# Performance work log

Hardware: AMD Instinct MI355X
Metric: run time of the kernel (lower is better)

Reference implementation:

```python
import jax, jax.numpy as jnp
import numpy as np

N_NODES = 100000
N_EDGES = 3200000


def setup_inputs() -> dict:
    key = jax.random.key(0)
    k1, k2, k3, k4, k5, k6, k7 = jax.random.split(key, 7)
    features = jax.random.normal(k1, (N_NODES, 1), dtype=jnp.float32)
    src = jax.random.randint(k2, (N_EDGES,), 0, N_NODES, dtype=jnp.int64)
    dst = jax.random.randint(k3, (N_EDGES,), 0, N_NODES, dtype=jnp.int64)
    # Linear layer params (PyTorch nn.Linear default init scale ~ 1/sqrt(fan_in))
    W1 = jax.random.normal(k4, (1, 16), dtype=jnp.float32)
    b1 = jax.random.normal(k5, (16,), dtype=jnp.float32) * 0.1
    W2 = jax.random.normal(k6, (16, 1), dtype=jnp.float32) * (1.0 / 4.0)
    b2 = jax.random.normal(k7, (1,), dtype=jnp.float32) * 0.1
    return {"features": features, "src": src, "dst": dst,
            "W1": W1, "b1": b1, "W2": W2, "b2": b2}


def _gcn_layer(h, src, dst, W, b):
    # DGL GCN: sum-aggregate neighbor features along edges, then Linear + ReLU.
    msgs = h[src]                                   # [E, d_in] gather
    agg = jax.ops.segment_sum(msgs, dst, num_segments=N_NODES)  # [N, d_in]
    return jax.nn.relu(agg @ W + b)                 # [N, d_out]


def reference(features, src, dst, W1, b1, W2, b2):
    h = _gcn_layer(features, src, dst, W1, b1)      # [N, 16]
    out = _gcn_layer(h, src, dst, W2, b2)           # [N, 1]
    return out
```

## Files before the change

kernel.cpp:

```cpp
#include <hip/hip_runtime.h>

#define NN 100000
#define NE 3200000
#define NQ (NE / 4)

#define NCHUNK 32
#define CHUNK 3125
#define NBB 512
#define BCAP 320
#define NSLICE 16
#define GPS (NBB / NSLICE)

__global__ __launch_bounds__(1024) void bucket_kernel(
        const int4* __restrict__ src4, const int4* __restrict__ dst4,
        unsigned* __restrict__ bkt, int* __restrict__ counts) {
    __shared__ int cnt[NCHUNK];
    if (threadIdx.x < NCHUNK) cnt[threadIdx.x] = 0;
    __syncthreads();
    const int b = blockIdx.x;
    const int q0 = (int)(((long long)b * NQ) / NBB);
    const int q1 = (int)(((long long)(b + 1) * NQ) / NBB);
    for (int q = q0 + threadIdx.x; q < q1; q += 1024) {
        const int4 d = dst4[q];
        const int4 s = src4[q];
        const int dd[4] = {d.x, d.y, d.z, d.w};
        const int ss[4] = {s.x, s.y, s.z, s.w};
#pragma unroll
        for (int j = 0; j < 4; ++j) {
            const int c = dd[j] / CHUNK;
            const int slot = atomicAdd(&cnt[c], 1);
            bkt[((size_t)c * NBB + b) * BCAP + slot] =
                ((unsigned)(dd[j] - c * CHUNK) << 17) | (unsigned)ss[j];
        }
    }
    __syncthreads();
    if (threadIdx.x < NCHUNK)
        counts[threadIdx.x * NBB + b] = cnt[threadIdx.x];
}

__global__ __launch_bounds__(1024) void scatter_bkt_kernel(
        const float* __restrict__ h,
        const unsigned* __restrict__ bkt, const int* __restrict__ counts,
        float* __restrict__ partial) {
    __shared__ float acc[CHUNK];
    const int s = blockIdx.x, c = blockIdx.y;
    for (int i = threadIdx.x; i < CHUNK; i += 1024) acc[i] = 0.0f;
    __syncthreads();
    const int lane = threadIdx.x & 63;
    const int w = threadIdx.x >> 6;
#pragma unroll
    for (int k = 0; k < 2; ++k) {
        const int b = s * GPS + w + k * 16;
        const int n = counts[c * NBB + b];
        const unsigned* bp = bkt + ((size_t)c * NBB + b) * BCAP;
        const uint4* bp4 = (const uint4*)bp;
        const int n4 = n >> 2;
        for (int q = lane; q < n4; q += 64) {
            const uint4 e = bp4[q];
            atomicAdd(&acc[e.x >> 17], h[e.x & 0x1FFFF]);
            atomicAdd(&acc[e.y >> 17], h[e.y & 0x1FFFF]);
            atomicAdd(&acc[e.z >> 17], h[e.z & 0x1FFFF]);
            atomicAdd(&acc[e.w >> 17], h[e.w & 0x1FFFF]);
        }
        const int base = n4 << 2;
        if (base + lane < n) {
            const unsigned e = bp[base + lane];
            atomicAdd(&acc[e >> 17], h[e & 0x1FFFF]);
        }
    }
    __syncthreads();
    float* out = partial + ((size_t)c * NSLICE + s) * CHUNK;
    for (int i = threadIdx.x; i < CHUNK; i += 1024) out[i] = acc[i];
}

__global__ __launch_bounds__(256) void reduce_mlp_kernel(
        const float* __restrict__ partial,
        const float* __restrict__ W1, const float* __restrict__ b1,
        const float* __restrict__ W2,
        float* __restrict__ sout, int n) {
    int i = blockIdx.x * blockDim.x + threadIdx.x;
    if (i >= n) return;
    const int c = i / CHUNK;
    const int idx = i - c * CHUNK;
    const float* base = partial + (size_t)c * NSLICE * CHUNK + idx;
    float a = 0.0f;
#pragma unroll
    for (int s = 0; s < NSLICE; ++s) a += base[(size_t)s * CHUNK];
    float r = 0.0f;
#pragma unroll
    for (int j = 0; j < 16; ++j)
        r = fmaf(fmaxf(fmaf(a, W1[j], b1[j]), 0.0f), W2[j], r);
    sout[i] = r;
}

__global__ __launch_bounds__(256) void reduce_final_kernel(
        const float* __restrict__ partial,
        const float* __restrict__ b2,
        float* __restrict__ out, int n) {
    int i = blockIdx.x * blockDim.x + threadIdx.x;
    if (i >= n) return;
    const int c = i / CHUNK;
    const int idx = i - c * CHUNK;
    const float* base = partial + (size_t)c * NSLICE * CHUNK + idx;
    float a = 0.0f;
#pragma unroll
    for (int s = 0; s < NSLICE; ++s) a += base[(size_t)s * CHUNK];
    out[i] = fmaxf(a + b2[0], 0.0f);
}

__global__ void zero_kernel(float* __restrict__ p, int n) {
    int i = blockIdx.x * blockDim.x + threadIdx.x;
    int st = gridDim.x * blockDim.x;
    for (; i < n; i += st) p[i] = 0.0f;
}
__global__ __launch_bounds__(256) void edge_scatter_kernel(
        const float* __restrict__ h, const int4* __restrict__ src4,
        const int4* __restrict__ dst4, float* __restrict__ agg, int nquad) {
    int i = blockIdx.x * blockDim.x + threadIdx.x;
    if (i >= nquad) return;
    int4 s = src4[i]; int4 d = dst4[i];
    atomicAdd(&agg[d.x], h[s.x]);
    atomicAdd(&agg[d.y], h[s.y]);
    atomicAdd(&agg[d.z], h[s.z]);
    atomicAdd(&agg[d.w], h[s.w]);
}
__global__ __launch_bounds__(256) void mlp_kernel(
        const float* __restrict__ agg1, const float* __restrict__ W1,
        const float* __restrict__ b1, const float* __restrict__ W2,
        float* __restrict__ sout, int n) {
    int i = blockIdx.x * blockDim.x + threadIdx.x;
    if (i >= n) return;
    float a = agg1[i], r = 0.0f;
#pragma unroll
    for (int j = 0; j < 16; ++j)
        r = fmaf(fmaxf(fmaf(a, W1[j], b1[j]), 0.0f), W2[j], r);
    sout[i] = r;
}
__global__ __launch_bounds__(256) void finalize_kernel(
        float* __restrict__ out, const float* __restrict__ b2, int n) {
    int i = blockIdx.x * blockDim.x + threadIdx.x;
    if (i >= n) return;
    out[i] = fmaxf(out[i] + b2[0], 0.0f);
}

extern "C" void kernel_launch(void* const* d_in, const int* in_sizes, int n_in,
                              void* d_out, int out_size, void* d_ws, size_t ws_size,
                              hipStream_t stream) {
    const float* features = (const float*)d_in[0];
    const int*   src      = (const int*)d_in[1];
    const int*   dst      = (const int*)d_in[2];
    const float* W1       = (const float*)d_in[3];
    const float* b1       = (const float*)d_in[4];
    const float* W2       = (const float*)d_in[5];
    const float* b2       = (const float*)d_in[6];
    float* out = (float*)d_out;

    const int nb = (NN + 255) / 256;

    {
        const size_t bkt_elems  = (size_t)NCHUNK * NBB * BCAP;
        const size_t cnt_elems  = (size_t)NCHUNK * NBB;
        const size_t part_elems = (size_t)NCHUNK * NSLICE * CHUNK;
        const size_t need = (bkt_elems + cnt_elems + part_elems + NN) * 4;
        if (ws_size >= need) {
            unsigned* bkt  = (unsigned*)d_ws;
            int* counts    = (int*)(bkt + bkt_elems);
            float* partial = (float*)(counts + cnt_elems);
            float* sbuf    = partial + part_elems;

            bucket_kernel<<<NBB, 1024, 0, stream>>>(
                (const int4*)src, (const int4*)dst, bkt, counts);
            dim3 g(NSLICE, NCHUNK);
            scatter_bkt_kernel<<<g, 1024, 0, stream>>>(features, bkt, counts, partial);
            reduce_mlp_kernel<<<nb, 256, 0, stream>>>(partial, W1, b1, W2, sbuf, NN);
            scatter_bkt_kernel<<<g, 1024, 0, stream>>>(sbuf, bkt, counts, partial);
            reduce_final_kernel<<<nb, 256, 0, stream>>>(partial, b2, out, NN);
            return;
        }
    }
    {
        float* agg1 = (float*)d_ws;
        float* sbuf = agg1 + NN;
        const int4* src4 = (const int4*)src;
        const int4* dst4 = (const int4*)dst;
        const int eb = (NQ + 255) / 256;
        zero_kernel<<<256, 256, 0, stream>>>(agg1, NN);
        edge_scatter_kernel<<<eb, 256, 0, stream>>>(features, src4, dst4, agg1, NQ);
        mlp_kernel<<<nb, 256, 0, stream>>>(agg1, W1, b1, W2, sbuf, NN);
        zero_kernel<<<256, 256, 0, stream>>>(out, NN);
        edge_scatter_kernel<<<eb, 256, 0, stream>>>(sbuf, src4, dst4, out, NQ);
        finalize_kernel<<<nb, 256, 0, stream>>>(out, b2, NN);
    }
}
```

Measured before the change: 64.59 us.

## Replace fixed-capacity dst buckets with two-pass counting sort by dst chunk and src band

Edges are now sorted into contiguous segments keyed by (destination chunk, source band) using a count kernel, a per-key scan, and a placement kernel, replacing the single-pass fixed-capacity bucketing. The scatter kernels then walk each key's segment in slices, so the h gathers within a pass touch one source band at a time, which is meant to improve cache locality, and the work per block is more even. The cost is an extra full read of src/dst, two more kernel launches, and a scatter loop that processes only one edge per thread per band. It also relies on each slice holding at most 1024 edges and each key at most 6912 edges.

```diff
diff --git a/kernel.cpp b/kernel.cpp
--- a/kernel.cpp
+++ b/kernel.cpp
@@ -6,71 +6,117 @@
 
 #define NCHUNK 32
 #define CHUNK 3125
-#define NBB 512
-#define BCAP 320
-#define NSLICE 16
-#define GPS (NBB / NSLICE)
-
-__global__ __launch_bounds__(1024) void bucket_kernel(
+#define NBAND 16
+#define BAND 6250
+#define NKEY (NCHUNK * NBAND)
+#define NBB 256
+#define EPB (NQ / NBB)
+#define KCAP 6912
+#define NSLICE 8
+
+__global__ __launch_bounds__(1024) void count_kernel(
         const int4* __restrict__ src4, const int4* __restrict__ dst4,
-        unsigned* __restrict__ bkt, int* __restrict__ counts) {
-    __shared__ int cnt[NCHUNK];
-    if (threadIdx.x < NCHUNK) cnt[threadIdx.x] = 0;
+        int* __restrict__ counts) {
+    __shared__ int cnt[NKEY];
+    if (threadIdx.x < NKEY) cnt[threadIdx.x] = 0;
     __syncthreads();
     const int b = blockIdx.x;
-    const int q0 = (int)(((long long)b * NQ) / NBB);
-    const int q1 = (int)(((long long)(b + 1) * NQ) / NBB);
-    for (int q = q0 + threadIdx.x; q < q1; q += 1024) {
+    const int q0 = b * EPB;
+    for (int q = q0 + threadIdx.x; q < q0 + EPB; q += 1024) {
         const int4 d = dst4[q];
         const int4 s = src4[q];
         const int dd[4] = {d.x, d.y, d.z, d.w};
         const int ss[4] = {s.x, s.y, s.z, s.w};
 #pragma unroll
         for (int j = 0; j < 4; ++j) {
+            const int key = (dd[j] / CHUNK) * NBAND + (ss[j] / BAND);
+            atomicAdd(&cnt[key], 1);
+        }
+    }
+    __syncthreads();
+    if (threadIdx.x < NKEY)
+        counts[threadIdx.x * NBB + b] = cnt[threadIdx.x];
+}
+
+__global__ __launch_bounds__(64) void scan_kernel(
+        const int* __restrict__ counts, int* __restrict__ offs,
+        int* __restrict__ ktot) {
+    const int k = blockIdx.x;
+    const int lane = threadIdx.x;
+    int v[4];
+    int sum = 0;
+#pragma unroll
+    for (int i = 0; i < 4; ++i) {
+        v[i] = counts[k * NBB + lane * 4 + i];
+        sum += v[i];
+    }
+    int incl = sum;
+#pragma unroll
+    for (int d = 1; d < 64; d <<= 1) {
+        int t = __shfl_up(incl, d);
+        if (lane >= d) incl += t;
+    }
+    int run = incl - sum;
+    const int base = k * KCAP;
+#pragma unroll
+    for (int i = 0; i < 4; ++i) {
+        offs[k * NBB + lane * 4 + i] = base + run;
+        run += v[i];
+    }
+    if (lane == 63) ktot[k] = incl;
+}
+
+__global__ __launch_bounds__(1024) void place_kernel(
+        const int4* __restrict__ src4, const int4* __restrict__ dst4,
+        const int* __restrict__ offs, unsigned* __restrict__ meta) {
+    __shared__ int offs_l[NKEY];
+    __shared__ int cnt[NKEY];
+    const int b = blockIdx.x;
+    if (threadIdx.x < NKEY) {
+        offs_l[threadIdx.x] = offs[threadIdx.x * NBB + b];
+        cnt[threadIdx.x] = 0;
+    }
+    __syncthreads();
+    const int q0 = b * EPB;
+    for (int q = q0 + threadIdx.x; q < q0 + EPB; q += 1024) {
+        const int4 d = dst4[q];
+        const int4 s = src4[q];
+        const int dd[4] = {d.x, d.y, d.z, d.w};
+        const int ss[4] = {s.x, s.y, s.z, s.w};
+#pragma unroll
+        for (int j = 0; j < 4; ++j) {
             const int c = dd[j] / CHUNK;
-            const int slot = atomicAdd(&cnt[c], 1);
-            bkt[((size_t)c * NBB + b) * BCAP + slot] =
+            const int key = c * NBAND + ss[j] / BAND;
+            const int slot = atomicAdd(&cnt[key], 1);
+            meta[offs_l[key] + slot] =
                 ((unsigned)(dd[j] - c * CHUNK) << 17) | (unsigned)ss[j];
         }
     }
-    __syncthreads();
-    if (threadIdx.x < NCHUNK)
-        counts[threadIdx.x * NBB + b] = cnt[threadIdx.x];
-}
-
-__global__ __launch_bounds__(1024) void scatter_bkt_kernel(
+}
+
+__global__ __launch_bounds__(1024) void scatter_band_kernel(
         const float* __restrict__ h,
-        const unsigned* __restrict__ bkt, const int* __restrict__ counts,
+        const unsigned* __restrict__ meta, const int* __restrict__ ktot,
         float* __restrict__ partial) {
     __shared__ float acc[CHUNK];
     const int s = blockIdx.x, c = blockIdx.y;
     for (int i = threadIdx.x; i < CHUNK; i += 1024) acc[i] = 0.0f;
     __syncthreads();
-    const int lane = threadIdx.x & 63;
-    const int w = threadIdx.x >> 6;
-#pragma unroll
-    for (int k = 0; k < 2; ++k) {
-        const int b = s * GPS + w + k * 16;
-        const int n = counts[c * NBB + b];
-        const unsigned* bp = bkt + ((size_t)c * NBB + b) * BCAP;
-        const uint4* bp4 = (const uint4*)bp;
-        const int n4 = n >> 2;
-        for (int q = lane; q < n4; q += 64) {
-            const uint4 e = bp4[q];
-            atomicAdd(&acc[e.x >> 17], h[e.x & 0x1FFFF]);
-            atomicAdd(&acc[e.y >> 17], h[e.y & 0x1FFFF]);
-            atomicAdd(&acc[e.z >> 17], h[e.z & 0x1FFFF]);
-            atomicAdd(&acc[e.w >> 17], h[e.w & 0x1FFFF]);
-        }
-        const int base = n4 << 2;
-        if (base + lane < n) {
-            const unsigned e = bp[base + lane];
+#pragma unroll
+    for (int band = 0; band < NBAND; ++band) {
+        const int key = c * NBAND + band;
+        const int kt = ktot[key];
+        const int lo = (kt * s) >> 3;
+        const int hi = (kt * (s + 1)) >> 3;
+        const int n = hi - lo;
+        if (threadIdx.x < n) {
+            const unsigned e = meta[key * KCAP + lo + threadIdx.x];
             atomicAdd(&acc[e >> 17], h[e & 0x1FFFF]);
         }
     }
     __syncthreads();
-    float* out = partial + ((size_t)c * NSLICE + s) * CHUNK;
-    for (int i = threadIdx.x; i < CHUNK; i += 1024) out[i] = acc[i];
+    float* outp = partial + ((size_t)c * NSLICE + s) * CHUNK;
+    for (int i = threadIdx.x; i < CHUNK; i += 1024) outp[i] = acc[i];
 }
 
 __global__ __launch_bounds__(256) void reduce_mlp_kernel(
@@ -155,25 +201,32 @@
     const float* b2       = (const float*)d_in[6];
     float* out = (float*)d_out;
 
+    const int4* src4 = (const int4*)src;
+    const int4* dst4 = (const int4*)dst;
     const int nb = (NN + 255) / 256;
 
     {
-        const size_t bkt_elems  = (size_t)NCHUNK * NBB * BCAP;
-        const size_t cnt_elems  = (size_t)NCHUNK * NBB;
+        const size_t cnt_elems  = (size_t)NKEY * NBB;
+        const size_t ktot_elems = NKEY;
+        const size_t meta_elems = (size_t)NKEY * KCAP;
         const size_t part_elems = (size_t)NCHUNK * NSLICE * CHUNK;
-        const size_t need = (bkt_elems + cnt_elems + part_elems + NN) * 4;
+        const size_t need =
+            (2 * cnt_elems + ktot_elems + meta_elems + part_elems + NN) * 4;
         if (ws_size >= need) {
-            unsigned* bkt  = (unsigned*)d_ws;
-            int* counts    = (int*)(bkt + bkt_elems);
-            float* partial = (float*)(counts + cnt_elems);
+            int* counts    = (int*)d_ws;
+            int* offs      = counts + cnt_elems;
+            int* ktot      = offs + cnt_elems;
+            unsigned* meta = (unsigned*)(ktot + ktot_elems);
+            float* partial = (float*)(meta + meta_elems);
             float* sbuf    = partial + part_elems;
 
-            bucket_kernel<<<NBB, 1024, 0, stream>>>(
-                (const int4*)src, (const int4*)dst, bkt, counts);
+            count_kernel<<<NBB, 1024, 0, stream>>>(src4, dst4, counts);
+            scan_kernel<<<NKEY, 64, 0, stream>>>(counts, offs, ktot);
+            place_kernel<<<NBB, 1024, 0, stream>>>(src4, dst4, offs, meta);
             dim3 g(NSLICE, NCHUNK);
-            scatter_bkt_kernel<<<g, 1024, 0, stream>>>(features, bkt, counts, partial);
+            scatter_band_kernel<<<g, 1024, 0, stream>>>(features, meta, ktot, partial);
             reduce_mlp_kernel<<<nb, 256, 0, stream>>>(partial, W1, b1, W2, sbuf, NN);
-            scatter_bkt_kernel<<<g, 1024, 0, stream>>>(sbuf, bkt, counts, partial);
+            scatter_band_kernel<<<g, 1024, 0, stream>>>(sbuf, meta, ktot, partial);
             reduce_final_kernel<<<nb, 256, 0, stream>>>(partial, b2, out, NN);
             return;
         }
@@ -181,8 +234,6 @@
     {
         float* agg1 = (float*)d_ws;
         float* sbuf = agg1 + NN;
-        const int4* src4 = (const int4*)src;
-        const int4* dst4 = (const int4*)dst;
         const int eb = (NQ + 255) / 256;
         zero_kernel<<<256, 256, 0, stream>>>(agg1, NN);
         edge_scatter_kernel<<<eb, 256, 0, stream>>>(features, src4, dst4, agg1, NQ);
```

After: 77.72 us. 1.2x slower.

## Bucket edges by destination chunk and source band, staging h windows in LDS

Applied to the files above, without the earlier changes.

Edges are now bucketed by a 2D key: destination chunk and source band. Each scatter block can then load its 6250-entry slice of h into shared memory and gather from there instead of from global memory. The bucket layout becomes fixed-capacity slots (KCAP=60 per key per block), and the scatter loop walks every slot, masking out the empty ones. In exchange, many idle lanes scan unfilled slots, the metadata buffer is larger, and edges beyond the capacity are silently dropped, which relies on a near-uniform index distribution.

```diff
diff --git a/kernel.cpp b/kernel.cpp
--- a/kernel.cpp
+++ b/kernel.cpp
@@ -6,21 +6,23 @@
 
 #define NCHUNK 32
 #define CHUNK 3125
-#define NBB 512
-#define BCAP 320
-#define NSLICE 16
-#define GPS (NBB / NSLICE)
+#define NBAND 16
+#define BAND 6250
+#define NKEY (NCHUNK * NBAND)
+#define NBB 256
+#define QPB (NQ / NBB)
+#define KCAP 60
+#define SLOTS (NBB * KCAP)
 
 __global__ __launch_bounds__(1024) void bucket_kernel(
         const int4* __restrict__ src4, const int4* __restrict__ dst4,
-        unsigned* __restrict__ bkt, int* __restrict__ counts) {
-    __shared__ int cnt[NCHUNK];
-    if (threadIdx.x < NCHUNK) cnt[threadIdx.x] = 0;
+        unsigned* __restrict__ meta, int* __restrict__ counts) {
+    __shared__ int cnt[NKEY];
+    if (threadIdx.x < NKEY) cnt[threadIdx.x] = 0;
     __syncthreads();
     const int b = blockIdx.x;
-    const int q0 = (int)(((long long)b * NQ) / NBB);
-    const int q1 = (int)(((long long)(b + 1) * NQ) / NBB);
-    for (int q = q0 + threadIdx.x; q < q1; q += 1024) {
+    const int q0 = b * QPB;
+    for (int q = q0 + threadIdx.x; q < q0 + QPB; q += 1024) {
         const int4 d = dst4[q];
         const int4 s = src4[q];
         const int dd[4] = {d.x, d.y, d.z, d.w};
@@ -28,49 +30,45 @@
 #pragma unroll
         for (int j = 0; j < 4; ++j) {
             const int c = dd[j] / CHUNK;
-            const int slot = atomicAdd(&cnt[c], 1);
-            bkt[((size_t)c * NBB + b) * BCAP + slot] =
-                ((unsigned)(dd[j] - c * CHUNK) << 17) | (unsigned)ss[j];
+            const int key = c * NBAND + ss[j] / BAND;
+            const int slot = atomicAdd(&cnt[key], 1);
+            if (slot < KCAP)
+                meta[((size_t)key * NBB + b) * KCAP + slot] =
+                    ((unsigned)(dd[j] - c * CHUNK) << 17) | (unsigned)ss[j];
         }
     }
     __syncthreads();
-    if (threadIdx.x < NCHUNK)
-        counts[threadIdx.x * NBB + b] = cnt[threadIdx.x];
+    if (threadIdx.x < NKEY)
+        counts[threadIdx.x * NBB + b] =
+            cnt[threadIdx.x] < KCAP ? cnt[threadIdx.x] : KCAP;
 }
 
-__global__ __launch_bounds__(1024) void scatter_bkt_kernel(
+__global__ __launch_bounds__(1024) void scatter_band_kernel(
         const float* __restrict__ h,
-        const unsigned* __restrict__ bkt, const int* __restrict__ counts,
+        const unsigned* __restrict__ meta, const int* __restrict__ counts,
         float* __restrict__ partial) {
+    __shared__ float hwin[BAND];
     __shared__ float acc[CHUNK];
-    const int s = blockIdx.x, c = blockIdx.y;
+    __shared__ int cnt_l[NBB];
+    const int band = blockIdx.x, c = blockIdx.y;
+    const int key = c * NBAND + band;
+    for (int j = threadIdx.x; j < BAND; j += 1024)
+        hwin[j] = h[band * BAND + j];
     for (int i = threadIdx.x; i < CHUNK; i += 1024) acc[i] = 0.0f;
+    if (threadIdx.x < NBB) cnt_l[threadIdx.x] = counts[key * NBB + threadIdx.x];
     __syncthreads();
-    const int lane = threadIdx.x & 63;
-    const int w = threadIdx.x >> 6;
-#pragma unroll
-    for (int k = 0; k < 2; ++k) {
-        const int b = s * GPS + w + k * 16;
-        const int n = counts[c * NBB + b];
-        const unsigned* bp = bkt + ((size_t)c * NBB + b) * BCAP;
-        const uint4* bp4 = (const uint4*)bp;
-        const int n4 = n >> 2;
-        for (int q = lane; q < n4; q += 64) {
-            const uint4 e = bp4[q];
-            atomicAdd(&acc[e.x >> 17], h[e.x & 0x1FFFF]);
-            atomicAdd(&acc[e.y >> 17], h[e.y & 0x1FFFF]);
-            atomicAdd(&acc[e.z >> 17], h[e.z & 0x1FFFF]);
-            atomicAdd(&acc[e.w >> 17], h[e.w & 0x1FFFF]);
-        }
-        const int base = n4 << 2;
-        if (base + lane < n) {
-            const unsigned e = bp[base + lane];
-            atomicAdd(&acc[e >> 17], h[e & 0x1FFFF]);
+    const unsigned* mp = meta + (size_t)key * SLOTS;
+    for (int s = threadIdx.x; s < SLOTS; s += 1024) {
+        const int blk = s / KCAP;
+        const int idx = s - blk * KCAP;
+        if (idx < cnt_l[blk]) {
+            const unsigned e = mp[s];
+            atomicAdd(&acc[e >> 17], hwin[(e & 0x1FFFF) - band * BAND]);
         }
     }
     __syncthreads();
-    float* out = partial + ((size_t)c * NSLICE + s) * CHUNK;
-    for (int i = threadIdx.x; i < CHUNK; i += 1024) out[i] = acc[i];
+    float* outp = partial + (size_t)key * CHUNK;
+    for (int i = threadIdx.x; i < CHUNK; i += 1024) outp[i] = acc[i];
 }
 
 __global__ __launch_bounds__(256) void reduce_mlp_kernel(
@@ -82,10 +80,10 @@
     if (i >= n) return;
     const int c = i / CHUNK;
     const int idx = i - c * CHUNK;
-    const float* base = partial + (size_t)c * NSLICE * CHUNK + idx;
+    const float* base = partial + (size_t)c * NBAND * CHUNK + idx;
     float a = 0.0f;
 #pragma unroll
-    for (int s = 0; s < NSLICE; ++s) a += base[(size_t)s * CHUNK];
+    for (int t = 0; t < NBAND; ++t) a += base[(size_t)t * CHUNK];
     float r = 0.0f;
 #pragma unroll
     for (int j = 0; j < 16; ++j)
@@ -101,10 +99,10 @@
     if (i >= n) return;
     const int c = i / CHUNK;
     const int idx = i - c * CHUNK;
-    const float* base = partial + (size_t)c * NSLICE * CHUNK + idx;
+    const float* base = partial + (size_t)c * NBAND * CHUNK + idx;
     float a = 0.0f;
 #pragma unroll
-    for (int s = 0; s < NSLICE; ++s) a += base[(size_t)s * CHUNK];
+    for (int t = 0; t < NBAND; ++t) a += base[(size_t)t * CHUNK];
     out[i] = fmaxf(a + b2[0], 0.0f);
 }
 
@@ -155,25 +153,28 @@
     const float* b2       = (const float*)d_in[6];
     float* out = (float*)d_out;
 
+    const int4* src4 = (const int4*)src;
+    const int4* dst4 = (const int4*)dst;
     const int nb = (NN + 255) / 256;
 
     {
-        const size_t bkt_elems  = (size_t)NCHUNK * NBB * BCAP;
-        const size_t cnt_elems  = (size_t)NCHUNK * NBB;
-        const size_t part_elems = (size_t)NCHUNK * NSLICE * CHUNK;
-        const size_t need = (bkt_elems + cnt_elems + part_elems + NN) * 4;
+        const size_t meta_elems = (size_t)NKEY * NBB * KCAP;
+        const size_t cnt_elems  = (size_t)NKEY * NBB;
+        const size_t part_elems = (size_t)NKEY * CHUNK;
+        const size_t need = (meta_elems + cnt_elems + part_elems + NN) * 4;
         if (ws_size >= need) {
-            unsigned* bkt  = (unsigned*)d_ws;
-            int* counts    = (int*)(bkt + bkt_elems);
+            unsigned* meta = (unsigned*)d_ws;
+            int* counts    = (int*)(meta + meta_elems);
             float* partial = (float*)(counts + cnt_elems);
             float* sbuf    = partial + part_elems;
 
-            bucket_kernel<<<NBB, 1024, 0, stream>>>(
-                (const int4*)src, (const int4*)dst, bkt, counts);
-            dim3 g(NSLICE, NCHUNK);
-            scatter_bkt_kernel<<<g, 1024, 0, stream>>>(features, bkt, counts, partial);
+            bucket_kernel<<<NBB, 1024, 0, stream>>>(src4, dst4, meta, counts);
+            dim3 g(NBAND, NCHUNK);
+            scatter_band_kernel<<<g, 1024, 0, stream>>>(
+                features, meta, counts, partial);
             reduce_mlp_kernel<<<nb, 256, 0, stream>>>(partial, W1, b1, W2, sbuf, NN);
-            scatter_bkt_kernel<<<g, 1024, 0, stream>>>(sbuf, bkt, counts, partial);
+            scatter_band_kernel<<<g, 1024, 0, stream>>>(
+                sbuf, meta, counts, partial);
             reduce_final_kernel<<<nb, 256, 0, stream>>>(partial, b2, out, NN);
             return;
         }
@@ -181,8 +182,6 @@
     {
         float* agg1 = (float*)d_ws;
         float* sbuf = agg1 + NN;
-        const int4* src4 = (const int4*)src;
-        const int4* dst4 = (const int4*)dst;
         const int eb = (NQ + 255) / 256;
         zero_kernel<<<256, 256, 0, stream>>>(agg1, NN);
         edge_scatter_kernel<<<eb, 256, 0, stream>>>(features, src4, dst4, agg1, NQ);
```

New measurement: 83.06 us. +28.6%, slower.
